# Performance work log

Hardware: AMD Instinct MI355X
Metric: run time of the kernel (lower is better)

## Reference

```python
import jax, jax.numpy as jnp
import numpy as np

B, S, D = 8, 1024, 1024
H, KV, HD = 16, 16, 64
NDIM = 2
EPS = 1e-6


def rms_norm(x, weight=None, eps=EPS):
    var = jnp.mean(jnp.square(x), axis=-1, keepdims=True)
    out = x * jax.lax.rsqrt(var + eps)
    if weight is not None:
        out = out * weight
    return out


def rotate_half(x):
    half = x.shape[-1] // 2
    return jnp.concatenate((-x[..., half:], x[..., :half]), axis=-1)


def multidim_rope(x, cos, sin, ndim):
    # x: [B,S,H,HD]; cos,sin: [B,S,HD]; head_dim split into ndim contiguous
    # chunks of size per = 2*(HD // (2*ndim)); rotate-half applied per chunk.
    b, s, h, hd = x.shape
    per = 2 * (hd // (2 * ndim))
    xg = x.reshape(b, s, h, ndim, per)
    cg = cos.reshape(b, s, 1, ndim, per)
    sg = sin.reshape(b, s, 1, ndim, per)
    out = xg * cg + rotate_half(xg) * sg
    return out.reshape(b, s, h, hd)


def setup_inputs() -> dict:
    key = jax.random.key(0)
    ks = jax.random.split(key, 10)
    scale = 1.0 / np.sqrt(D)
    return {
        "hidden_states": jax.random.normal(ks[0], (B, S, D), jnp.float32),
        "cos": jax.random.uniform(ks[1], (B, S, HD), jnp.float32, -1.0, 1.0),
        "sin": jax.random.uniform(ks[2], (B, S, HD), jnp.float32, -1.0, 1.0),
        "position_ids": jax.random.randint(ks[3], (B, S, NDIM), 0, 32, jnp.int32),
        "wq": jax.random.normal(ks[4], (D, H * HD), jnp.float32) * scale,
        "wk": jax.random.normal(ks[5], (D, KV * HD), jnp.float32) * scale,
        "wv": jax.random.normal(ks[6], (D, KV * HD), jnp.float32) * scale,
        "wo": jax.random.normal(ks[7], (H * HD, D), jnp.float32) * scale,
        "q_norm_w": jnp.ones((HD,), jnp.float32),
        "k_norm_w": jnp.ones((HD,), jnp.float32),
    }


def reference(hidden_states, cos, sin, position_ids, wq, wk, wv, wo, q_norm_w, k_norm_w):
    b, s, _ = hidden_states.shape
    ndim = position_ids.shape[-1]

    q = (hidden_states @ wq).reshape(b, s, H, HD)
    q = rms_norm(q, q_norm_w)
    q = multidim_rope(q, cos, sin, ndim)

    k = (hidden_states @ wk).reshape(b, s, KV, HD)
    k = rms_norm(k, k_norm_w)
    k = multidim_rope(k, cos, sin, ndim)

    v = (hidden_states @ wv).reshape(b, s, KV, HD)
    v = rms_norm(v, None)  # v_norm has no weight

    # Full (non-causal) vision attention, scaling = 1.0
    scores = jnp.einsum("bqhd,bkhd->bhqk", q, k)
    probs = jax.nn.softmax(scores, axis=-1)
    attn = jnp.einsum("bhqk,bkhd->bqhd", probs, v).reshape(b, s, H * HD)

    return attn @ wo
```

## Files before the change

### kernel.cpp

```cpp
#include <hip/hip_runtime.h>
#include <hip/hip_bf16.h>

typedef __attribute__((ext_vector_type(8))) short bf16x8;
typedef __attribute__((ext_vector_type(4))) short bf16x4;
typedef __attribute__((ext_vector_type(4))) float f32x4;

struct __align__(16) V16 { unsigned long long a, b; };

__device__ __forceinline__ float bf2f(unsigned short u) {
  union { unsigned int i; float f; } c; c.i = ((unsigned int)u) << 16; return c.f;
}
__device__ __forceinline__ unsigned short f2bf(float f) {
  unsigned int u; __builtin_memcpy(&u, &f, 4);
  u += 0x7FFFu + ((u >> 16) & 1u);
  return (unsigned short)(u >> 16);
}

__device__ __forceinline__ void async16(unsigned short* lds,
                                        const unsigned short* g) {
  __builtin_amdgcn_global_load_lds(
      (const __attribute__((address_space(1))) unsigned int*)g,
      (__attribute__((address_space(3))) unsigned int*)lds, 16, 0, 0);
}

__device__ __forceinline__ void xcd_swizzle(int& bx, int& by) {
  const int nx = (int)gridDim.x;
  const int nwg = nx * (int)gridDim.y;
  if ((nwg & 7) == 0) {
    int orig = by * nx + bx;
    int swz = (orig & 7) * (nwg >> 3) + (orig >> 3);
    bx = swz % nx;
    by = swz / nx;
  }
}

#define FP32_MAGIC 0x3F800000u

__device__ __forceinline__ void cvt_seg(
    const void* __restrict__ src, unsigned short* __restrict__ dst,
    int n4, int i, int stride, bool f32)
{
  if (f32) {
    const float* s = (const float*)src;
    for (; i < n4; i += stride) {
      float4 v = *(const float4*)(s + (size_t)i * 4);
      ushort2 lo = { f2bf(v.x), f2bf(v.y) };
      ushort2 hi = { f2bf(v.z), f2bf(v.w) };
      *(ushort2*)(dst + (size_t)i * 4)     = lo;
      *(ushort2*)(dst + (size_t)i * 4 + 2) = hi;
    }
  } else {
    const unsigned short* s = (const unsigned short*)src;
    for (; i < n4; i += stride)
      *(ushort4*)(dst + (size_t)i * 4) = *(const ushort4*)(s + (size_t)i * 4);
  }
}

__global__ __launch_bounds__(256) void cvt_bf16(
    const void* __restrict__ src, size_t srcOff,
    unsigned short* __restrict__ dst, int n4,
    const unsigned int* __restrict__ fmt)
{
  const bool f32 = (fmt[0] == FP32_MAGIC);
  const int i = blockIdx.x * blockDim.x + threadIdx.x;
  const int stride = gridDim.x * blockDim.x;
  const void* s = f32 ? (const void*)((const float*)src + srcOff)
                      : (const void*)((const unsigned short*)src + srcOff);
  cvt_seg(s, dst, n4, i, stride, f32);
}

__global__ __launch_bounds__(256) void cvt_all(
    const void* __restrict__ hid, const void* __restrict__ cosr,
    const void* __restrict__ sinr, const void* __restrict__ qnw,
    const void* __restrict__ knw,
    unsigned short* __restrict__ hb, unsigned short* __restrict__ csb,
    unsigned short* __restrict__ snb, unsigned short* __restrict__ qnb,
    unsigned short* __restrict__ knb,
    int hidden_n4, const unsigned int* __restrict__ fmt)
{
  const bool f32 = (fmt[0] == FP32_MAGIC);
  const int bx = blockIdx.x, tid = threadIdx.x;
  if (bx < 2048) {
    if (hidden_n4 > 0)
      cvt_seg(hid, hb, hidden_n4, bx * 256 + tid, 2048 * 256, f32);
  } else if (bx < 2176) {
    cvt_seg(cosr, csb, 131072, (bx - 2048) * 256 + tid, 128 * 256, f32);
  } else if (bx < 2304) {
    cvt_seg(sinr, snb, 131072, (bx - 2176) * 256 + tid, 128 * 256, f32);
  } else {
    if (tid < 16)       cvt_seg(qnw, qnb, 16, tid, 16, f32);
    else if (tid < 32)  cvt_seg(knw, knb, 16, tid - 16, 16, f32);
  }
}

__global__ __launch_bounds__(256) void cvt_t4(
    const void* __restrict__ s0, const void* __restrict__ s1,
    const void* __restrict__ s2, const void* __restrict__ s3,
    unsigned short* __restrict__ d0, unsigned short* __restrict__ d1,
    unsigned short* __restrict__ d2, unsigned short* __restrict__ d3,
    const unsigned int* __restrict__ fmt)
{
  __shared__ __align__(16) unsigned short T[64][72];
  const int z = blockIdx.z;
  const void* src = (z == 0) ? s0 : (z == 1) ? s1 : (z == 2) ? s2 : s3;
  unsigned short* dstT = (z == 0) ? d0 : (z == 1) ? d1 : (z == 2) ? d2 : d3;

  const bool f32 = (fmt[0] == FP32_MAGIC);
  const int tid = threadIdx.x;
  const int k0 = blockIdx.x * 64, n0 = blockIdx.y * 64;
  const int rl = tid >> 3, cl = (tid & 7) * 8;

#pragma unroll
  for (int p = 0; p < 2; ++p) {
    int r = rl + p * 32;
    int cs = cl ^ (r & 56);
    if (f32) {
      const float* s = (const float*)src + (size_t)(k0 + r) * 1024 + n0 + cl;
      float4 v0 = *(const float4*)s, v1 = *(const float4*)(s + 4);
      unsigned short* t = &T[r][cs];
      t[0]=f2bf(v0.x); t[1]=f2bf(v0.y); t[2]=f2bf(v0.z); t[3]=f2bf(v0.w);
      t[4]=f2bf(v1.x); t[5]=f2bf(v1.y); t[6]=f2bf(v1.z); t[7]=f2bf(v1.w);
    } else {
      *(V16*)&T[r][cs] = *(const V16*)((const unsigned short*)src +
                                        (size_t)(k0 + r) * 1024 + n0 + cl);
    }
  }
  __syncthreads();

#pragma unroll
  for (int p = 0; p < 2; ++p) {
    int u = tid + p * 256;
    int d = u >> 3, sc = (u & 7) * 8;
    unsigned short tmp[8];
#pragma unroll
    for (int i = 0; i < 8; ++i) tmp[i] = T[sc + i][d ^ sc];
    *(V16*)&dstT[(size_t)(n0 + d) * 1024 + k0 + sc] = *(V16*)tmp;
  }
}

#define TK 64
#define GK 1024
#define QTM 256
#define QTN 128

__global__ __launch_bounds__(512, 2) void gemm_qkv(
    const unsigned short* __restrict__ A,
    const unsigned short* __restrict__ Bt,
    unsigned short* __restrict__ Cq,
    unsigned short* __restrict__ Ck,
    unsigned short* __restrict__ Cv,
    const unsigned short* __restrict__ cs,
    const unsigned short* __restrict__ sn,
    const unsigned short* __restrict__ qw,
    const unsigned short* __restrict__ kw,
    int M)
{
  __shared__ __align__(16) unsigned short LDSu[2 * (QTM + QTN) * TK];

  const int tid  = threadIdx.x;
  const int wave = tid >> 6;
  const int lane = tid & 63;
  const int quad = lane >> 4;
  const int l16  = lane & 15;
  const int wr   = wave >> 1;
  const int wc   = wave & 1;
  const int bm = blockIdx.x * QTM;
  const int bn = blockIdx.y * QTN;

  const f32x4 z = {0.f, 0.f, 0.f, 0.f};
  f32x4 acc[4][4];
#pragma unroll
  for (int i = 0; i < 4; ++i)
#pragma unroll
    for (int j = 0; j < 4; ++j) acc[i][j] = z;

  const int lrow = lane >> 3;
  const int gcol = ((lane & 7) ^ lrow) * 8;
  const unsigned short* aP = A  + (size_t)(bm + wave * 8 + lrow) * GK + gcol;
  const unsigned short* bP = Bt + (size_t)(bn + wave * 8 + lrow) * GK + gcol;
  const int cswz = l16 & 7;

  unsigned short* As0 = LDSu;
  unsigned short* Bs0 = LDSu + QTM * TK;
  const int BUFS = (QTM + QTN) * TK;

  auto STAGE_A = [&](int b, int t, int p) {
    async16(As0 + b * BUFS + (p * 64 + wave * 8) * TK,
            aP + (size_t)(p * 64) * GK + t * TK);
  };
  auto STAGE_B = [&](int b, int t, int p) {
    async16(Bs0 + b * BUFS + (p * 64 + wave * 8) * TK,
            bP + (size_t)(p * 64) * GK + t * TK);
  };

  STAGE_A(0, 0, 0); STAGE_A(0, 0, 1); STAGE_A(0, 0, 2); STAGE_A(0, 0, 3);
  STAGE_B(0, 0, 0); STAGE_B(0, 0, 1);

#pragma unroll 2
  for (int t = 0; t < 16; ++t) {
    const int cur = t & 1, nxt = cur ^ 1;

    if (t < 15) {
      STAGE_A(nxt, t + 1, 0); STAGE_A(nxt, t + 1, 1); STAGE_B(nxt, t + 1, 0);
      asm volatile("s_waitcnt vmcnt(3)" ::: "memory");
    } else {
      asm volatile("s_waitcnt vmcnt(0)" ::: "memory");
    }
    asm volatile("s_barrier" ::: "memory");

    const unsigned short* Ab = As0 + cur * BUFS;
    const unsigned short* Bb = Bs0 + cur * BUFS;
    bf16x8 af[4][2], bfv[4][2];
#pragma unroll
    for (int ks = 0; ks < 2; ++ks) {
      const int pc = ((ks * 4 + quad) ^ cswz) * 8;
#pragma unroll
      for (int mt = 0; mt < 4; ++mt)
        af[mt][ks] = *(const bf16x8*)&Ab[(wr * 64 + mt * 16 + l16) * TK + pc];
#pragma unroll
      for (int nt = 0; nt < 4; ++nt)
        bfv[nt][ks] = *(const bf16x8*)&Bb[(wc * 64 + nt * 16 + l16) * TK + pc];
    }

    __builtin_amdgcn_s_setprio(1);
#pragma unroll
    for (int mt = 0; mt < 4; ++mt)
#pragma unroll
      for (int nt = 0; nt < 4; ++nt)
        acc[mt][nt] = __builtin_amdgcn_mfma_f32_16x16x32_bf16(
            af[mt][0], bfv[nt][0], acc[mt][nt], 0, 0, 0);
    __builtin_amdgcn_s_setprio(0);
    asm volatile("s_barrier" ::: "memory");

    if (t < 15) {
      STAGE_A(nxt, t + 1, 2); STAGE_A(nxt, t + 1, 3); STAGE_B(nxt, t + 1, 1);
    }
    __builtin_amdgcn_s_setprio(1);
#pragma unroll
    for (int mt = 0; mt < 4; ++mt)
#pragma unroll
      for (int nt = 0; nt < 4; ++nt)
        acc[mt][nt] = __builtin_amdgcn_mfma_f32_16x16x32_bf16(
            af[mt][1], bfv[nt][1], acc[mt][nt], 0, 0, 0);
    __builtin_amdgcn_s_setprio(0);
    asm volatile("s_barrier" ::: "memory");
  }

  const int which = bn >> 10;
  const int colbase = (bn & 1023) + wc * 64;

  if (which == 2) {
    unsigned short* Tw = LDSu + wave * 4096;
#pragma unroll
    for (int mt = 0; mt < 4; ++mt)
#pragma unroll
      for (int r = 0; r < 4; ++r) {
        const int s = mt * 16 + quad * 4 + r;
        float x0 = acc[mt][0][r], x1 = acc[mt][1][r];
        float x2 = acc[mt][2][r], x3 = acc[mt][3][r];
        float ss = x0 * x0 + x1 * x1 + x2 * x2 + x3 * x3;
        ss += __shfl_xor(ss, 1);
        ss += __shfl_xor(ss, 2);
        ss += __shfl_xor(ss, 4);
        ss += __shfl_xor(ss, 8);
        const float inv = rsqrtf(ss * (1.f / 64.f) + 1e-6f);
        const int sw = (s >> 3) << 3;
#pragma unroll
        for (int nt = 0; nt < 4; ++nt)
          Tw[s * 64 + ((nt * 16 + l16) ^ sw)] = f2bf(acc[mt][nt][r] * inv);
      }
    __builtin_amdgcn_wave_barrier();

    const int vhead = ((bm >> 10) * 16 + (colbase >> 6)) * 64;
    const int sbase = (bm & 1023) + wr * 64;
    const int sg = (lane & 7) * 8;
    const int dl = lane >> 3;
#pragma unroll
    for (int p = 0; p < 8; ++p) {
      const int d = p * 8 + dl;
      unsigned short tmp[8];
#pragma unroll
      for (int i = 0; i < 8; ++i)
        tmp[i] = Tw[(sg + i) * 64 + (d ^ sg)];
      *(V16*)&Cv[(size_t)(vhead + d) * 1024 + sbase + sg] = *(V16*)tmp;
    }
    return;
  }

  unsigned short* Cd = (which == 0) ? Cq : Ck;
  float wgt[4];
#pragma unroll
  for (int nt = 0; nt < 4; ++nt) {
    int d = nt * 16 + l16;
    wgt[nt] = (which == 0) ? bf2f(qw[d]) * 1.44269504f : bf2f(kw[d]);
  }

#pragma unroll
  for (int mt = 0; mt < 4; ++mt)
#pragma unroll
    for (int r = 0; r < 4; ++r) {
      const int row = bm + wr * 64 + mt * 16 + quad * 4 + r;
      float x0 = acc[mt][0][r], x1 = acc[mt][1][r];
      float x2 = acc[mt][2][r], x3 = acc[mt][3][r];
      float ss = x0 * x0 + x1 * x1 + x2 * x2 + x3 * x3;
      ss += __shfl_xor(ss, 1);
      ss += __shfl_xor(ss, 2);
      ss += __shfl_xor(ss, 4);
      ss += __shfl_xor(ss, 8);
      const float inv = rsqrtf(ss * (1.f / 64.f) + 1e-6f);
      float y[4] = { x0 * inv * wgt[0], x1 * inv * wgt[1],
                     x2 * inv * wgt[2], x3 * inv * wgt[3] };
      const unsigned short* cp = cs + (size_t)row * 64 + l16;
      const unsigned short* sp = sn + (size_t)row * 64 + l16;
#pragma unroll
      for (int nt = 0; nt < 4; ++nt) {
        float c = bf2f(cp[nt * 16]), s = bf2f(sp[nt * 16]);
        float part = (nt & 1) ? y[nt ^ 1] : -y[nt ^ 1];
        Cd[(size_t)row * 1024 + colbase + nt * 16 + l16] =
            f2bf(y[nt] * c + part * s);
      }
    }
}

#define TM 128
#define TN 128

__global__ __launch_bounds__(256) void gemm_bf16(
    const unsigned short* __restrict__ A,
    const unsigned short* __restrict__ Bt,
    void* __restrict__ C, size_t cOff,
    const unsigned int* __restrict__ outFmt,
    int M, int N)
{
  __shared__ __align__(16) unsigned short As[TM][TK];
  __shared__ __align__(16) unsigned short Bs[TN][TK];

  const int tid  = threadIdx.x;
  const int wave = tid >> 6;
  const int lane = tid & 63;
  const int quad = lane >> 4;
  const int l16  = lane & 15;
  const int bm = blockIdx.x * TM;
  const int bn = blockIdx.y * TN;
  const int wm = (wave & 1) * 64;
  const int wn = (wave >> 1) * 64;

  const f32x4 z = {0.f, 0.f, 0.f, 0.f};
  f32x4 acc[4][4];
#pragma unroll
  for (int i = 0; i < 4; ++i)
#pragma unroll
    for (int j = 0; j < 4; ++j) acc[i][j] = z;

  const int lrow = lane >> 3;
  const int gcol = ((lane & 7) ^ lrow) * 8;
  const unsigned short* aP = A  + (size_t)(bm + wave * 8 + lrow) * GK + gcol;
  const unsigned short* bP = Bt + (size_t)(bn + wave * 8 + lrow) * GK + gcol;
  const int cswz = l16 & 7;

  for (int k0 = 0; k0 < GK; k0 += TK) {
#pragma unroll
    for (int p = 0; p < 4; ++p) {
      async16(&As[p * 32 + wave * 8][0], aP + (size_t)p * 32 * GK);
      async16(&Bs[p * 32 + wave * 8][0], bP + (size_t)p * 32 * GK);
    }
    aP += TK; bP += TK;
    __syncthreads();

#pragma unroll
    for (int s = 0; s < 2; ++s) {
      const int pc = ((s * 4 + quad) ^ cswz) * 8;
      bf16x8 af[4], bfv[4];
#pragma unroll
      for (int mt = 0; mt < 4; ++mt)
        af[mt] = *(const bf16x8*)&As[wm + mt * 16 + l16][pc];
#pragma unroll
      for (int nt = 0; nt < 4; ++nt)
        bfv[nt] = *(const bf16x8*)&Bs[wn + nt * 16 + l16][pc];
#pragma unroll
      for (int mt = 0; mt < 4; ++mt)
#pragma unroll
        for (int nt = 0; nt < 4; ++nt)
          acc[mt][nt] = __builtin_amdgcn_mfma_f32_16x16x32_bf16(
              af[mt], bfv[nt], acc[mt][nt], 0, 0, 0);
    }
    __syncthreads();
  }

  const bool of32 = (outFmt != nullptr) && (outFmt[0] == FP32_MAGIC);
  float* Cf = (float*)C + cOff;
  unsigned short* Ch = (unsigned short*)C + cOff;

#pragma unroll
  for (int mt = 0; mt < 4; ++mt)
#pragma unroll
    for (int nt = 0; nt < 4; ++nt)
#pragma unroll
      for (int r = 0; r < 4; ++r) {
        int row = bm + wm + mt * 16 + quad * 4 + r;
        int col = bn + wn + nt * 16 + l16;
        size_t idx = (size_t)row * N + col;
        if (of32) Cf[idx] = acc[mt][nt][r];
        else      Ch[idx] = f2bf(acc[mt][nt][r]);
      }
}

__global__ __launch_bounds__(256, 3) void attn_fused(
    const unsigned short* __restrict__ q,
    const unsigned short* __restrict__ k,
    const unsigned short* __restrict__ vt,
    unsigned short* __restrict__ o)
{
  __shared__ __align__(16) unsigned short Ks[2][64][64];
  __shared__ __align__(16) unsigned short Vs[2][64][64];

  int bxs = blockIdx.x, bys = blockIdx.y;
  xcd_swizzle(bxs, bys);

  const int tid  = threadIdx.x;
  const int wave = tid >> 6;
  const int lane = tid & 63;
  const int quad = lane >> 4;
  const int l16  = lane & 15;
  const int bh = bys;
  const int b  = bh >> 4, h = bh & 15;
  const int qbase = bxs * 128 + wave * 32;
  const size_t bbase = (size_t)b * 1024;

  bf16x8 qfA[2], qfB[2];
  {
    const unsigned short* qp = q + (bbase + qbase + l16) * 1024 + h * 64;
    qfA[0] = *(const bf16x8*)(qp + quad * 8);
    qfA[1] = *(const bf16x8*)(qp + 32 + quad * 8);
    qfB[0] = *(const bf16x8*)(qp + 16 * 1024 + quad * 8);
    qfB[1] = *(const bf16x8*)(qp + 16 * 1024 + 32 + quad * 8);
  }

  const f32x4 z = {0.f, 0.f, 0.f, 0.f};
  f32x4 ofA[5], ofB[5];
#pragma unroll
  for (int nt = 0; nt < 5; ++nt) { ofA[nt] = z; ofB[nt] = z; }
  float mA = -1e30f, mB = -1e30f;

  const bf16x8 onesv = { 0x3F80, 0x3F80, 0x3F80, 0x3F80,
                         0x3F80, 0x3F80, 0x3F80, 0x3F80 };

  const int lrow = lane >> 3;
  const int gcol = ((lane & 7) ^ lrow) * 8;
  const unsigned short* kP = k  + (bbase + wave * 8 + lrow) * 1024 + h * 64 + gcol;
  const unsigned short* vP = vt + ((size_t)bh * 64 + wave * 8 + lrow) * 1024 + gcol;
  const int cswz = l16 & 7;

  auto STAGE = [&](int buf, int kt) {
#pragma unroll
    for (int p = 0; p < 2; ++p) {
      async16(&Ks[buf][p * 32 + wave * 8][0], kP + ((size_t)kt * 64 + p * 32) * 1024);
      async16(&Vs[buf][p * 32 + wave * 8][0], vP + (size_t)p * 32 * 1024 + kt * 64);
    }
  };

  STAGE(0, 0);
  __syncthreads();

#pragma unroll 2
  for (int kt = 0; kt < 16; ++kt) {
    const int cur = kt & 1;
    if (kt < 15) STAGE(cur ^ 1, kt + 1);

    f32x4 sA[4], sB[4];
#pragma unroll
    for (int nt = 0; nt < 4; ++nt) { sA[nt] = z; sB[nt] = z; }
    __builtin_amdgcn_s_setprio(1);
#pragma unroll
    for (int s = 0; s < 2; ++s) {
      const int pc = ((s * 4 + quad) ^ cswz) * 8;
#pragma unroll
      for (int nt = 0; nt < 4; ++nt) {
        bf16x8 kf = *(const bf16x8*)&Ks[cur][nt * 16 + l16][pc];
        sA[nt] = __builtin_amdgcn_mfma_f32_16x16x32_bf16(kf, qfA[s], sA[nt], 0, 0, 0);
        sB[nt] = __builtin_amdgcn_mfma_f32_16x16x32_bf16(kf, qfB[s], sB[nt], 0, 0, 0);
      }
    }
    __builtin_amdgcn_s_setprio(0);

    float mxA, mxB;
    {
      float a0 = fmaxf(fmaxf(sA[0][0], sA[0][1]), fmaxf(sA[0][2], sA[0][3]));
      float a1 = fmaxf(fmaxf(sA[1][0], sA[1][1]), fmaxf(sA[1][2], sA[1][3]));
      float a2 = fmaxf(fmaxf(sA[2][0], sA[2][1]), fmaxf(sA[2][2], sA[2][3]));
      float a3 = fmaxf(fmaxf(sA[3][0], sA[3][1]), fmaxf(sA[3][2], sA[3][3]));
      mxA = fmaxf(fmaxf(a0, a1), fmaxf(a2, a3));
      mxA = fmaxf(mxA, __shfl_xor(mxA, 16));
      mxA = fmaxf(mxA, __shfl_xor(mxA, 32));
      float b0 = fmaxf(fmaxf(sB[0][0], sB[0][1]), fmaxf(sB[0][2], sB[0][3]));
      float b1 = fmaxf(fmaxf(sB[1][0], sB[1][1]), fmaxf(sB[1][2], sB[1][3]));
      float b2 = fmaxf(fmaxf(sB[2][0], sB[2][1]), fmaxf(sB[2][2], sB[2][3]));
      float b3 = fmaxf(fmaxf(sB[3][0], sB[3][1]), fmaxf(sB[3][2], sB[3][3]));
      mxB = fmaxf(fmaxf(b0, b1), fmaxf(b2, b3));
      mxB = fmaxf(mxB, __shfl_xor(mxB, 16));
      mxB = fmaxf(mxB, __shfl_xor(mxB, 32));
    }

    if (!__all((mxA - mA <= 11.5f) && (mxB - mB <= 11.5f))) {
      float mnA = fmaxf(mA, mxA);
      float mnB = fmaxf(mB, mxB);
      float aA = __builtin_amdgcn_exp2f(mA - mnA);
      float aB = __builtin_amdgcn_exp2f(mB - mnB);
      mA = mnA; mB = mnB;
      float arA[4], arB[4];
#pragma unroll
      for (int r = 0; r < 4; ++r) {
        arA[r] = __shfl(aA, quad * 4 + r);
        arB[r] = __shfl(aB, quad * 4 + r);
      }
#pragma unroll
      for (int nt = 0; nt < 5; ++nt)
#pragma unroll
        for (int r = 0; r < 4; ++r) {
          ofA[nt][r] *= arA[r];
          ofB[nt][r] *= arB[r];
        }
    }

    bf16x8 pA[2], pB[2];
#pragma unroll
    for (int nt = 0; nt < 4; ++nt)
#pragma unroll
      for (int r = 0; r < 4; ++r) {
        pA[nt >> 1][(nt & 1) * 4 + r] =
            (short)f2bf(__builtin_amdgcn_exp2f(sA[nt][r] - mA));
        pB[nt >> 1][(nt & 1) * 4 + r] =
            (short)f2bf(__builtin_amdgcn_exp2f(sB[nt][r] - mB));
      }

    __builtin_amdgcn_s_setprio(1);
#pragma unroll
    for (int s = 0; s < 2; ++s) {
#pragma unroll
      for (int nt = 0; nt < 4; ++nt) {
        const unsigned short* vrow = &Vs[cur][nt * 16 + l16][0];
        const int g0  = (4 * s + (quad >> 1)) ^ cswz;
        const int off = 4 * (quad & 1);
        bf16x4 v0 = *(const bf16x4*)(vrow + g0 * 8 + off);
        bf16x4 v1 = *(const bf16x4*)(vrow + (g0 ^ 2) * 8 + off);
        bf16x8 vf = __builtin_shufflevector(v0, v1, 0, 1, 2, 3, 4, 5, 6, 7);
        ofA[nt] = __builtin_amdgcn_mfma_f32_16x16x32_bf16(pA[s], vf, ofA[nt], 0, 0, 0);
        ofB[nt] = __builtin_amdgcn_mfma_f32_16x16x32_bf16(pB[s], vf, ofB[nt], 0, 0, 0);
      }
      ofA[4] = __builtin_amdgcn_mfma_f32_16x16x32_bf16(pA[s], onesv, ofA[4], 0, 0, 0);
      ofB[4] = __builtin_amdgcn_mfma_f32_16x16x32_bf16(pB[s], onesv, ofB[4], 0, 0, 0);
    }
    __builtin_amdgcn_s_setprio(0);

    __syncthreads();
  }

  float ilA[4], ilB[4];
#pragma unroll
  for (int r = 0; r < 4; ++r) {
    ilA[r] = 1.f / ofA[4][r];
    ilB[r] = 1.f / ofB[4][r];
  }
#pragma unroll
  for (int nt = 0; nt < 4; ++nt)
#pragma unroll
    for (int r = 0; r < 4; ++r) {
      int row = qbase + quad * 4 + r;
      o[(bbase + row) * 1024 + h * 64 + nt * 16 + l16] = f2bf(ofA[nt][r] * ilA[r]);
      o[(bbase + row + 16) * 1024 + h * 64 + nt * 16 + l16] = f2bf(ofB[nt][r] * ilB[r]);
    }
}

extern "C" void kernel_launch(void* const* d_in, const int* in_sizes, int n_in,
                              void* d_out, int out_size, void* d_ws, size_t ws_size,
                              hipStream_t stream) {
  const void* hidden = d_in[0];
  const void* cosr   = d_in[1];
  const void* sinr   = d_in[2];
  const void* wq     = d_in[4];
  const void* wk     = d_in[5];
  const void* wv     = d_in[6];
  const void* wo     = d_in[7];
  const void* qnw    = d_in[8];
  const void* knw    = d_in[9];
  const unsigned int* fmt = (const unsigned int*)qnw;

  const size_t MEG = 1024 * 1024;
  dim3 blk(256);
  dim3 blk512(512);
  unsigned short* w = (unsigned short*)d_ws;

  if (ws_size >= (size_t)60 * MEG) {
    unsigned short* hb   = w;
    unsigned short* wqT  = w + 8 * MEG;
    unsigned short* wkT  = w + 9 * MEG;
    unsigned short* wvT  = w + 10 * MEG;
    unsigned short* woT  = w + 11 * MEG;
    unsigned short* csb  = w + 12 * MEG;
    unsigned short* snb  = w + 12 * MEG + 512 * 1024;
    unsigned short* qnb  = w + 13 * MEG;
    unsigned short* knb  = w + 13 * MEG + 64;
    unsigned short* qb   = w + 14 * MEG;
    unsigned short* kb   = w + 22 * MEG;
    unsigned short* vtb  = (unsigned short*)d_out;
    unsigned short* ab   = qb;

    cvt_all<<<dim3(2305), blk, 0, stream>>>(hidden, cosr, sinr, qnw, knw,
                                            hb, csb, snb, qnb, knb,
                                            2 * (int)MEG, fmt);
    cvt_t4<<<dim3(16, 16, 4), blk, 0, stream>>>(wq, wk, wv, wo,
                                                wqT, wkT, wvT, woT, fmt);

    const int M = 8192;
    gemm_qkv<<<dim3(M / QTM, 24), blk512, 0, stream>>>(hb, wqT, qb, kb, vtb,
                                                       csb, snb, qnb, knb, M);
    attn_fused<<<dim3(8, 8 * 16), blk, 0, stream>>>(qb, kb, vtb, ab);
    gemm_bf16<<<dim3(M / TM, 8), blk, 0, stream>>>(ab, woT, d_out, 0, fmt,
                                                   M, 1024);
  } else {
    unsigned short* wqT  = w;
    unsigned short* wkT  = w + 1 * MEG;
    unsigned short* wvT  = w + 2 * MEG;
    unsigned short* woT  = w + 3 * MEG;
    unsigned short* csb  = w + 4 * MEG;
    unsigned short* snb  = w + 4 * MEG + 512 * 1024;
    unsigned short* qnb  = w + 5 * MEG;
    unsigned short* knb  = w + 5 * MEG + 64;
    unsigned short* hbb  = w + 6 * MEG;
    unsigned short* qb   = w + 7 * MEG;
    unsigned short* kb   = w + 8 * MEG;
    unsigned short* vtb  = w + 10 * MEG;

    cvt_t4<<<dim3(16, 16, 4), blk, 0, stream>>>(wq, wk, wv, wo,
                                                wqT, wkT, wvT, woT, fmt);
    cvt_all<<<dim3(2305), blk, 0, stream>>>(hidden, cosr, sinr, qnw, knw,
                                            nullptr, csb, snb, qnb, knb,
                                            0, fmt);

    const int Mb = 1024;
    for (int b = 0; b < 8; ++b) {
      cvt_bf16<<<dim3(512), blk, 0, stream>>>(hidden, (size_t)b * MEG, hbb,
                                              (int)(MEG / 4), fmt);
      gemm_qkv<<<dim3(Mb / QTM, 24), blk512, 0, stream>>>(
          hbb, wqT, qb, kb, vtb, csb + (size_t)b * 64 * 1024,
          snb + (size_t)b * 64 * 1024, qnb, knb, Mb);
      attn_fused<<<dim3(8, 16), blk, 0, stream>>>(qb, kb, vtb, qb);
      gemm_bf16<<<dim3(Mb / TM, 8), blk, 0, stream>>>(qb, woT, d_out,
                                                      (size_t)b * MEG, fmt,
                                                      Mb, 1024);
    }
  }
}
```

Before: 251.7 us.

## Double-buffer output projection GEMM with 512 threads; permute V^T stores for single-load V fragments

The output projection GEMM moves to 512-thread blocks with QTM×QTN tiles and double-buffered LDS. Async global-to-LDS loads for the next K tile are split across two phases and overlap the MFMA work, using explicit vmcnt waits and raw barriers instead of __syncthreads. The QKV epilogue now writes V^T with a permuted sequence layout, so the attention kernel can read each V fragment with one 16-byte LDS load instead of two 8-byte loads and a shuffle. This trades more LDS and hand-written synchronisation for better latency hiding, and both kernels must agree exactly on the permuted layout.

Result: no change. 255.6 us (+1.5%).

```diff
diff --git a/kernel.cpp b/kernel.cpp
--- a/kernel.cpp
+++ b/kernel.cpp
@@ -273,16 +273,22 @@
 
     const int vhead = ((bm >> 10) * 16 + (colbase >> 6)) * 64;
     const int sbase = (bm & 1023) + wr * 64;
-    const int sg = (lane & 7) * 8;
+    const int c  = lane & 7;
+    const int sg = c * 8;
     const int dl = lane >> 3;
+    const int m0 = 2 * c, m1 = 2 * c + 1;
+    const int P0 = 32 * (m0 >> 3) + 8 * (m0 & 3) + 4 * ((m0 >> 2) & 1);
+    const int P1 = 32 * (m1 >> 3) + 8 * (m1 & 3) + 4 * ((m1 >> 2) & 1);
 #pragma unroll
     for (int p = 0; p < 8; ++p) {
       const int d = p * 8 + dl;
-      unsigned short tmp[8];
+      union { unsigned short u[8]; unsigned long long q[2]; } tmp;
 #pragma unroll
       for (int i = 0; i < 8; ++i)
-        tmp[i] = Tw[(sg + i) * 64 + (d ^ sg)];
-      *(V16*)&Cv[(size_t)(vhead + d) * 1024 + sbase + sg] = *(V16*)tmp;
+        tmp.u[i] = Tw[(sg + i) * 64 + (d ^ sg)];
+      unsigned short* dst = &Cv[(size_t)(vhead + d) * 1024 + sbase];
+      *(unsigned long long*)(dst + P0) = tmp.q[0];
+      *(unsigned long long*)(dst + P1) = tmp.q[1];
     }
     return;
   }
@@ -322,28 +328,24 @@
     }
 }
 
-#define TM 128
-#define TN 128
-
-__global__ __launch_bounds__(256) void gemm_bf16(
+__global__ __launch_bounds__(512, 2) void gemm_bf16(
     const unsigned short* __restrict__ A,
     const unsigned short* __restrict__ Bt,
     void* __restrict__ C, size_t cOff,
     const unsigned int* __restrict__ outFmt,
     int M, int N)
 {
-  __shared__ __align__(16) unsigned short As[TM][TK];
-  __shared__ __align__(16) unsigned short Bs[TN][TK];
+  __shared__ __align__(16) unsigned short LDSu[2 * (QTM + QTN) * TK];
 
   const int tid  = threadIdx.x;
   const int wave = tid >> 6;
   const int lane = tid & 63;
   const int quad = lane >> 4;
   const int l16  = lane & 15;
-  const int bm = blockIdx.x * TM;
-  const int bn = blockIdx.y * TN;
-  const int wm = (wave & 1) * 64;
-  const int wn = (wave >> 1) * 64;
+  const int wr   = wave >> 1;
+  const int wc   = wave & 1;
+  const int bm = blockIdx.x * QTM;
+  const int bn = blockIdx.y * QTN;
 
   const f32x4 z = {0.f, 0.f, 0.f, 0.f};
   f32x4 acc[4][4];
@@ -358,33 +360,70 @@
   const unsigned short* bP = Bt + (size_t)(bn + wave * 8 + lrow) * GK + gcol;
   const int cswz = l16 & 7;
 
-  for (int k0 = 0; k0 < GK; k0 += TK) {
-#pragma unroll
-    for (int p = 0; p < 4; ++p) {
-      async16(&As[p * 32 + wave * 8][0], aP + (size_t)p * 32 * GK);
-      async16(&Bs[p * 32 + wave * 8][0], bP + (size_t)p * 32 * GK);
-    }
-    aP += TK; bP += TK;
-    __syncthreads();
-
-#pragma unroll
-    for (int s = 0; s < 2; ++s) {
-      const int pc = ((s * 4 + quad) ^ cswz) * 8;
-      bf16x8 af[4], bfv[4];
+  unsigned short* As0 = LDSu;
+  unsigned short* Bs0 = LDSu + QTM * TK;
+  const int BUFS = (QTM + QTN) * TK;
+
+  auto STAGE_A = [&](int b, int t, int p) {
+    async16(As0 + b * BUFS + (p * 64 + wave * 8) * TK,
+            aP + (size_t)(p * 64) * GK + t * TK);
+  };
+  auto STAGE_B = [&](int b, int t, int p) {
+    async16(Bs0 + b * BUFS + (p * 64 + wave * 8) * TK,
+            bP + (size_t)(p * 64) * GK + t * TK);
+  };
+
+  STAGE_A(0, 0, 0); STAGE_A(0, 0, 1); STAGE_A(0, 0, 2); STAGE_A(0, 0, 3);
+  STAGE_B(0, 0, 0); STAGE_B(0, 0, 1);
+
+#pragma unroll 2
+  for (int t = 0; t < 16; ++t) {
+    const int cur = t & 1, nxt = cur ^ 1;
+
+    if (t < 15) {
+      STAGE_A(nxt, t + 1, 0); STAGE_A(nxt, t + 1, 1); STAGE_B(nxt, t + 1, 0);
+      asm volatile("s_waitcnt vmcnt(3)" ::: "memory");
+    } else {
+      asm volatile("s_waitcnt vmcnt(0)" ::: "memory");
+    }
+    asm volatile("s_barrier" ::: "memory");
+
+    const unsigned short* Ab = As0 + cur * BUFS;
+    const unsigned short* Bb = Bs0 + cur * BUFS;
+    bf16x8 af[4][2], bfv[4][2];
+#pragma unroll
+    for (int ks = 0; ks < 2; ++ks) {
+      const int pc = ((ks * 4 + quad) ^ cswz) * 8;
 #pragma unroll
       for (int mt = 0; mt < 4; ++mt)
-        af[mt] = *(const bf16x8*)&As[wm + mt * 16 + l16][pc];
+        af[mt][ks] = *(const bf16x8*)&Ab[(wr * 64 + mt * 16 + l16) * TK + pc];
 #pragma unroll
       for (int nt = 0; nt < 4; ++nt)
-        bfv[nt] = *(const bf16x8*)&Bs[wn + nt * 16 + l16][pc];
-#pragma unroll
-      for (int mt = 0; mt < 4; ++mt)
-#pragma unroll
-        for (int nt = 0; nt < 4; ++nt)
-          acc[mt][nt] = __builtin_amdgcn_mfma_f32_16x16x32_bf16(
-              af[mt], bfv[nt], acc[mt][nt], 0, 0, 0);
-    }
-    __syncthreads();
+        bfv[nt][ks] = *(const bf16x8*)&Bb[(wc * 64 + nt * 16 + l16) * TK + pc];
+    }
+
+    __builtin_amdgcn_s_setprio(1);
+#pragma unroll
+    for (int mt = 0; mt < 4; ++mt)
+#pragma unroll
+      for (int nt = 0; nt < 4; ++nt)
+        acc[mt][nt] = __builtin_amdgcn_mfma_f32_16x16x32_bf16(
+            af[mt][0], bfv[nt][0], acc[mt][nt], 0, 0, 0);
+    __builtin_amdgcn_s_setprio(0);
+    asm volatile("s_barrier" ::: "memory");
+
+    if (t < 15) {
+      STAGE_A(nxt, t + 1, 2); STAGE_A(nxt, t + 1, 3); STAGE_B(nxt, t + 1, 1);
+    }
+    __builtin_amdgcn_s_setprio(1);
+#pragma unroll
+    for (int mt = 0; mt < 4; ++mt)
+#pragma unroll
+      for (int nt = 0; nt < 4; ++nt)
+        acc[mt][nt] = __builtin_amdgcn_mfma_f32_16x16x32_bf16(
+            af[mt][1], bfv[nt][1], acc[mt][nt], 0, 0, 0);
+    __builtin_amdgcn_s_setprio(0);
+    asm volatile("s_barrier" ::: "memory");
   }
 
   const bool of32 = (outFmt != nullptr) && (outFmt[0] == FP32_MAGIC);
@@ -397,8 +436,8 @@
     for (int nt = 0; nt < 4; ++nt)
 #pragma unroll
       for (int r = 0; r < 4; ++r) {
-        int row = bm + wm + mt * 16 + quad * 4 + r;
-        int col = bn + wn + nt * 16 + l16;
+        int row = bm + wr * 64 + mt * 16 + quad * 4 + r;
+        int col = bn + wc * 64 + nt * 16 + l16;
         size_t idx = (size_t)row * N + col;
         if (of32) Cf[idx] = acc[mt][nt][r];
         else      Ch[idx] = f2bf(acc[mt][nt][r]);
@@ -536,14 +575,10 @@
     __builtin_amdgcn_s_setprio(1);
 #pragma unroll
     for (int s = 0; s < 2; ++s) {
+      const int pc = ((s * 4 + quad) ^ cswz) * 8;
 #pragma unroll
       for (int nt = 0; nt < 4; ++nt) {
-        const unsigned short* vrow = &Vs[cur][nt * 16 + l16][0];
-        const int g0  = (4 * s + (quad >> 1)) ^ cswz;
-        const int off = 4 * (quad & 1);
-        bf16x4 v0 = *(const bf16x4*)(vrow + g0 * 8 + off);
-        bf16x4 v1 = *(const bf16x4*)(vrow + (g0 ^ 2) * 8 + off);
-        bf16x8 vf = __builtin_shufflevector(v0, v1, 0, 1, 2, 3, 4, 5, 6, 7);
+        bf16x8 vf = *(const bf16x8*)&Vs[cur][nt * 16 + l16][pc];
         ofA[nt] = __builtin_amdgcn_mfma_f32_16x16x32_bf16(pA[s], vf, ofA[nt], 0, 0, 0);
         ofB[nt] = __builtin_amdgcn_mfma_f32_16x16x32_bf16(pB[s], vf, ofB[nt], 0, 0, 0);
       }
@@ -615,8 +650,8 @@
     gemm_qkv<<<dim3(M / QTM, 24), blk512, 0, stream>>>(hb, wqT, qb, kb, vtb,
                                                        csb, snb, qnb, knb, M);
     attn_fused<<<dim3(8, 8 * 16), blk, 0, stream>>>(qb, kb, vtb, ab);
-    gemm_bf16<<<dim3(M / TM, 8), blk, 0, stream>>>(ab, woT, d_out, 0, fmt,
-                                                   M, 1024);
+    gemm_bf16<<<dim3(M / QTM, 8), blk512, 0, stream>>>(ab, woT, d_out, 0, fmt,
+                                                       M, 1024);
   } else {
     unsigned short* wqT  = w;
     unsigned short* wkT  = w + 1 * MEG;
@@ -645,9 +680,9 @@
           hbb, wqT, qb, kb, vtb, csb + (size_t)b * 64 * 1024,
           snb + (size_t)b * 64 * 1024, qnb, knb, Mb);
       attn_fused<<<dim3(8, 16), blk, 0, stream>>>(qb, kb, vtb, qb);
-      gemm_bf16<<<dim3(Mb / TM, 8), blk, 0, stream>>>(qb, woT, d_out,
-                                                      (size_t)b * MEG, fmt,
-                                                      Mb, 1024);
-    }
-  }
-}
+      gemm_bf16<<<dim3(Mb / QTM, 8), blk512, 0, stream>>>(qb, woT, d_out,
+                                                          (size_t)b * MEG, fmt,
+                                                          Mb, 1024);
+    }
+  }
+}
```

## Enlarge QKV GEMM tile to 256x256 and permute V-transpose store layout

Applied to the files above, without the earlier changes.

The fused QKV projection GEMM tile grows from 256x128 to 256x256, with waves rearranged 2x4 so each wave computes 128x64. This raises arithmetic intensity per LDS load and halves the grid in N. The V epilogue now writes transposed V in a permuted sequence order, and attention loads V fragments as a single 16-byte read instead of two 8-byte reads plus a shuffle. Risks are higher register pressure from doubled accumulators, fewer blocks per CU, and correctness hinging on the V permutation matching the attention kernel's P fragment order.

After: 300.6 us. 19.4% more time.

```diff
diff --git a/kernel.cpp b/kernel.cpp
--- a/kernel.cpp
+++ b/kernel.cpp
@@ -141,7 +141,7 @@
 #define TK 64
 #define GK 1024
 #define QTM 256
-#define QTN 128
+#define QTN 256
 
 __global__ __launch_bounds__(512, 2) void gemm_qkv(
     const unsigned short* __restrict__ A,
@@ -162,15 +162,15 @@
   const int lane = tid & 63;
   const int quad = lane >> 4;
   const int l16  = lane & 15;
-  const int wr   = wave >> 1;
-  const int wc   = wave & 1;
+  const int wr   = wave >> 2;
+  const int wc   = wave & 3;
   const int bm = blockIdx.x * QTM;
   const int bn = blockIdx.y * QTN;
 
   const f32x4 z = {0.f, 0.f, 0.f, 0.f};
-  f32x4 acc[4][4];
-#pragma unroll
-  for (int i = 0; i < 4; ++i)
+  f32x4 acc[8][4];
+#pragma unroll
+  for (int i = 0; i < 8; ++i)
 #pragma unroll
     for (int j = 0; j < 4; ++j) acc[i][j] = z;
 
@@ -194,15 +194,16 @@
   };
 
   STAGE_A(0, 0, 0); STAGE_A(0, 0, 1); STAGE_A(0, 0, 2); STAGE_A(0, 0, 3);
-  STAGE_B(0, 0, 0); STAGE_B(0, 0, 1);
+  STAGE_B(0, 0, 0); STAGE_B(0, 0, 1); STAGE_B(0, 0, 2); STAGE_B(0, 0, 3);
 
 #pragma unroll 2
   for (int t = 0; t < 16; ++t) {
     const int cur = t & 1, nxt = cur ^ 1;
 
     if (t < 15) {
-      STAGE_A(nxt, t + 1, 0); STAGE_A(nxt, t + 1, 1); STAGE_B(nxt, t + 1, 0);
-      asm volatile("s_waitcnt vmcnt(3)" ::: "memory");
+      STAGE_A(nxt, t + 1, 0); STAGE_A(nxt, t + 1, 1);
+      STAGE_B(nxt, t + 1, 0); STAGE_B(nxt, t + 1, 1);
+      asm volatile("s_waitcnt vmcnt(4)" ::: "memory");
     } else {
       asm volatile("s_waitcnt vmcnt(0)" ::: "memory");
     }
@@ -210,39 +211,50 @@
 
     const unsigned short* Ab = As0 + cur * BUFS;
     const unsigned short* Bb = Bs0 + cur * BUFS;
-    bf16x8 af[4][2], bfv[4][2];
-#pragma unroll
-    for (int ks = 0; ks < 2; ++ks) {
-      const int pc = ((ks * 4 + quad) ^ cswz) * 8;
-#pragma unroll
-      for (int mt = 0; mt < 4; ++mt)
-        af[mt][ks] = *(const bf16x8*)&Ab[(wr * 64 + mt * 16 + l16) * TK + pc];
+
+    {
+      const int pc = (quad ^ cswz) * 8;
+      bf16x8 af[8], bfv[4];
+#pragma unroll
+      for (int mt = 0; mt < 8; ++mt)
+        af[mt] = *(const bf16x8*)&Ab[(wr * 128 + mt * 16 + l16) * TK + pc];
 #pragma unroll
       for (int nt = 0; nt < 4; ++nt)
-        bfv[nt][ks] = *(const bf16x8*)&Bb[(wc * 64 + nt * 16 + l16) * TK + pc];
-    }
-
-    __builtin_amdgcn_s_setprio(1);
-#pragma unroll
-    for (int mt = 0; mt < 4; ++mt)
+        bfv[nt] = *(const bf16x8*)&Bb[(wc * 64 + nt * 16 + l16) * TK + pc];
+      __builtin_amdgcn_s_setprio(1);
+#pragma unroll
+      for (int mt = 0; mt < 8; ++mt)
+#pragma unroll
+        for (int nt = 0; nt < 4; ++nt)
+          acc[mt][nt] = __builtin_amdgcn_mfma_f32_16x16x32_bf16(
+              af[mt], bfv[nt], acc[mt][nt], 0, 0, 0);
+      __builtin_amdgcn_s_setprio(0);
+    }
+    asm volatile("s_barrier" ::: "memory");
+
+    if (t < 15) {
+      STAGE_A(nxt, t + 1, 2); STAGE_A(nxt, t + 1, 3);
+      STAGE_B(nxt, t + 1, 2); STAGE_B(nxt, t + 1, 3);
+    }
+
+    {
+      const int pc = ((4 + quad) ^ cswz) * 8;
+      bf16x8 af[8], bfv[4];
+#pragma unroll
+      for (int mt = 0; mt < 8; ++mt)
+        af[mt] = *(const bf16x8*)&Ab[(wr * 128 + mt * 16 + l16) * TK + pc];
 #pragma unroll
       for (int nt = 0; nt < 4; ++nt)
-        acc[mt][nt] = __builtin_amdgcn_mfma_f32_16x16x32_bf16(
-            af[mt][0], bfv[nt][0], acc[mt][nt], 0, 0, 0);
-    __builtin_amdgcn_s_setprio(0);
-    asm volatile("s_barrier" ::: "memory");
-
-    if (t < 15) {
-      STAGE_A(nxt, t + 1, 2); STAGE_A(nxt, t + 1, 3); STAGE_B(nxt, t + 1, 1);
-    }
-    __builtin_amdgcn_s_setprio(1);
-#pragma unroll
-    for (int mt = 0; mt < 4; ++mt)
-#pragma unroll
-      for (int nt = 0; nt < 4; ++nt)
-        acc[mt][nt] = __builtin_amdgcn_mfma_f32_16x16x32_bf16(
-            af[mt][1], bfv[nt][1], acc[mt][nt], 0, 0, 0);
-    __builtin_amdgcn_s_setprio(0);
+        bfv[nt] = *(const bf16x8*)&Bb[(wc * 64 + nt * 16 + l16) * TK + pc];
+      __builtin_amdgcn_s_setprio(1);
+#pragma unroll
+      for (int mt = 0; mt < 8; ++mt)
+#pragma unroll
+        for (int nt = 0; nt < 4; ++nt)
+          acc[mt][nt] = __builtin_amdgcn_mfma_f32_16x16x32_bf16(
+              af[mt], bfv[nt], acc[mt][nt], 0, 0, 0);
+      __builtin_amdgcn_s_setprio(0);
+    }
     asm volatile("s_barrier" ::: "memory");
   }
 
@@ -251,38 +263,49 @@
 
   if (which == 2) {
     unsigned short* Tw = LDSu + wave * 4096;
-#pragma unroll
-    for (int mt = 0; mt < 4; ++mt)
-#pragma unroll
-      for (int r = 0; r < 4; ++r) {
-        const int s = mt * 16 + quad * 4 + r;
-        float x0 = acc[mt][0][r], x1 = acc[mt][1][r];
-        float x2 = acc[mt][2][r], x3 = acc[mt][3][r];
-        float ss = x0 * x0 + x1 * x1 + x2 * x2 + x3 * x3;
-        ss += __shfl_xor(ss, 1);
-        ss += __shfl_xor(ss, 2);
-        ss += __shfl_xor(ss, 4);
-        ss += __shfl_xor(ss, 8);
-        const float inv = rsqrtf(ss * (1.f / 64.f) + 1e-6f);
-        const int sw = (s >> 3) << 3;
-#pragma unroll
-        for (int nt = 0; nt < 4; ++nt)
-          Tw[s * 64 + ((nt * 16 + l16) ^ sw)] = f2bf(acc[mt][nt][r] * inv);
+    const int vhead = ((bm >> 10) * 16 + (colbase >> 6)) * 64;
+    const int c  = lane & 7;
+    const int sg = c * 8;
+    const int dl = lane >> 3;
+    const int m0 = 2 * c, m1 = 2 * c + 1;
+    const int P0 = 32 * (m0 >> 3) + 8 * (m0 & 3) + 4 * ((m0 >> 2) & 1);
+    const int P1 = 32 * (m1 >> 3) + 8 * (m1 & 3) + 4 * ((m1 >> 2) & 1);
+
+#pragma unroll
+    for (int h2 = 0; h2 < 2; ++h2) {
+#pragma unroll
+      for (int mt = 0; mt < 4; ++mt)
+#pragma unroll
+        for (int r = 0; r < 4; ++r) {
+          const int s = mt * 16 + quad * 4 + r;
+          const f32x4* a = &acc[h2 * 4 + mt][0];
+          float x0 = a[0][r], x1 = a[1][r], x2 = a[2][r], x3 = a[3][r];
+          float ss = x0 * x0 + x1 * x1 + x2 * x2 + x3 * x3;
+          ss += __shfl_xor(ss, 1);
+          ss += __shfl_xor(ss, 2);
+          ss += __shfl_xor(ss, 4);
+          ss += __shfl_xor(ss, 8);
+          const float inv = rsqrtf(ss * (1.f / 64.f) + 1e-6f);
+          const int sw = (s >> 3) << 3;
+#pragma unroll
+          for (int nt = 0; nt < 4; ++nt)
+            Tw[s * 64 + ((nt * 16 + l16) ^ sw)] = f2bf(a[nt][r] * inv);
+        }
+      __builtin_amdgcn_wave_barrier();
+
+      const int sbase = (bm & 1023) + wr * 128 + h2 * 64;
+#pragma unroll
+      for (int p = 0; p < 8; ++p) {
+        const int d = p * 8 + dl;
+        union { unsigned short u[8]; unsigned long long q[2]; } tmp;
+#pragma unroll
+        for (int i = 0; i < 8; ++i)
+          tmp.u[i] = Tw[(sg + i) * 64 + (d ^ sg)];
+        unsigned short* dst = &Cv[(size_t)(vhead + d) * 1024 + sbase];
+        *(unsigned long long*)(dst + P0) = tmp.q[0];
+        *(unsigned long long*)(dst + P1) = tmp.q[1];
       }
-    __builtin_amdgcn_wave_barrier();
-
-    const int vhead = ((bm >> 10) * 16 + (colbase >> 6)) * 64;
-    const int sbase = (bm & 1023) + wr * 64;
-    const int sg = (lane & 7) * 8;
-    const int dl = lane >> 3;
-#pragma unroll
-    for (int p = 0; p < 8; ++p) {
-      const int d = p * 8 + dl;
-      unsigned short tmp[8];
-#pragma unroll
-      for (int i = 0; i < 8; ++i)
-        tmp[i] = Tw[(sg + i) * 64 + (d ^ sg)];
-      *(V16*)&Cv[(size_t)(vhead + d) * 1024 + sbase + sg] = *(V16*)tmp;
+      __builtin_amdgcn_wave_barrier();
     }
     return;
   }
@@ -296,10 +319,10 @@
   }
 
 #pragma unroll
-  for (int mt = 0; mt < 4; ++mt)
+  for (int mt = 0; mt < 8; ++mt)
 #pragma unroll
     for (int r = 0; r < 4; ++r) {
-      const int row = bm + wr * 64 + mt * 16 + quad * 4 + r;
+      const int row = bm + wr * 128 + mt * 16 + quad * 4 + r;
       float x0 = acc[mt][0][r], x1 = acc[mt][1][r];
       float x2 = acc[mt][2][r], x3 = acc[mt][3][r];
       float ss = x0 * x0 + x1 * x1 + x2 * x2 + x3 * x3;
@@ -536,14 +559,10 @@
     __builtin_amdgcn_s_setprio(1);
 #pragma unroll
     for (int s = 0; s < 2; ++s) {
+      const int pc = ((s * 4 + quad) ^ cswz) * 8;
 #pragma unroll
       for (int nt = 0; nt < 4; ++nt) {
-        const unsigned short* vrow = &Vs[cur][nt * 16 + l16][0];
-        const int g0  = (4 * s + (quad >> 1)) ^ cswz;
-        const int off = 4 * (quad & 1);
-        bf16x4 v0 = *(const bf16x4*)(vrow + g0 * 8 + off);
-        bf16x4 v1 = *(const bf16x4*)(vrow + (g0 ^ 2) * 8 + off);
-        bf16x8 vf = __builtin_shufflevector(v0, v1, 0, 1, 2, 3, 4, 5, 6, 7);
+        bf16x8 vf = *(const bf16x8*)&Vs[cur][nt * 16 + l16][pc];
         ofA[nt] = __builtin_amdgcn_mfma_f32_16x16x32_bf16(pA[s], vf, ofA[nt], 0, 0, 0);
         ofB[nt] = __builtin_amdgcn_mfma_f32_16x16x32_bf16(pB[s], vf, ofB[nt], 0, 0, 0);
       }
@@ -612,7 +631,7 @@
                                                 wqT, wkT, wvT, woT, fmt);
 
     const int M = 8192;
-    gemm_qkv<<<dim3(M / QTM, 24), blk512, 0, stream>>>(hb, wqT, qb, kb, vtb,
+    gemm_qkv<<<dim3(M / QTM, 12), blk512, 0, stream>>>(hb, wqT, qb, kb, vtb,
                                                        csb, snb, qnb, knb, M);
     attn_fused<<<dim3(8, 8 * 16), blk, 0, stream>>>(qb, kb, vtb, ab);
     gemm_bf16<<<dim3(M / TM, 8), blk, 0, stream>>>(ab, woT, d_out, 0, fmt,
@@ -641,7 +660,7 @@
     for (int b = 0; b < 8; ++b) {
       cvt_bf16<<<dim3(512), blk, 0, stream>>>(hidden, (size_t)b * MEG, hbb,
                                               (int)(MEG / 4), fmt);
-      gemm_qkv<<<dim3(Mb / QTM, 24), blk512, 0, stream>>>(
+      gemm_qkv<<<dim3(Mb / QTM, 12), blk512, 0, stream>>>(
           hbb, wqT, qb, kb, vtb, csb + (size_t)b * 64 * 1024,
           snb + (size_t)b * 64 * 1024, qnb, knb, Mb);
       attn_fused<<<dim3(8, 16), blk, 0, stream>>>(qb, kb, vtb, qb);
```
